# Kernel optimization log

Measured on AMD Instinct MI355X. Metric: run time of the kernel, lower is better.

Reference implementation:

```python
import jax, jax.numpy as jnp
import numpy as np

N = 50000      # nodes
E = 800000     # edges (before self-loops)
IN = 256       # in_channels
HID = 128      # hidden_channels
OUT = 128      # out_channels
NEG_SLOPE = 0.2
EPS = 1e-16


def setup_inputs() -> dict:
    key = jax.random.key(0)
    ks = jax.random.split(key, 16)
    p = lambda k, shape: jax.random.normal(k, shape, jnp.float32) * 0.1
    return {
        "x": jax.random.normal(ks[0], (N, IN), jnp.float32),
        "edge_index": jax.random.randint(ks[1], (2, E), 0, N, dtype=jnp.int64),
        # semantic MLP
        "W1": p(ks[2], (IN, HID)), "b1": jnp.zeros((HID,), jnp.float32),
        "W2": p(ks[3], (HID, HID)), "b2": jnp.zeros((HID,), jnp.float32),
        # gat1: HID -> HID//2, heads=4, concat -> 2*HID
        "g1_W": p(ks[4], (HID, 4 * (HID // 2))),
        "g1_as": p(ks[5], (4, HID // 2)), "g1_ad": p(ks[6], (4, HID // 2)),
        "g1_b": jnp.zeros((4 * (HID // 2),), jnp.float32),
        # gat2: 2*HID -> OUT, heads=2, mean -> OUT
        "g2_W": p(ks[7], (2 * HID, 2 * OUT)),
        "g2_as": p(ks[8], (2, OUT)), "g2_ad": p(ks[9], (2, OUT)),
        "g2_b": jnp.zeros((OUT,), jnp.float32),
        # gat3: OUT -> OUT, heads=1, mean -> OUT
        "g3_W": p(ks[10], (OUT, OUT)),
        "g3_as": p(ks[11], (1, OUT)), "g3_ad": p(ks[12], (1, OUT)),
        "g3_b": jnp.zeros((OUT,), jnp.float32),
    }


def _gat(h_in, src, dst, W, a_src, a_dst, bias, heads, concat, n):
    # Linear projection into heads: [n, H, C]
    h = (h_in @ W).reshape(n, heads, -1)
    alpha_s = jnp.sum(h * a_src[None], axis=-1)  # [n, H]
    alpha_d = jnp.sum(h * a_dst[None], axis=-1)  # [n, H]
    e = jax.nn.leaky_relu(alpha_s[src] + alpha_d[dst], NEG_SLOPE)  # [E', H]
    # segment softmax over edges grouped by destination node
    m = jax.ops.segment_max(e, dst, num_segments=n)
    ex = jnp.exp(e - m[dst])
    denom = jax.ops.segment_sum(ex, dst, num_segments=n)
    alpha = ex / (denom[dst] + EPS)  # [E', H]
    msg = h[src] * alpha[..., None]  # [E', H, C]
    out = jax.ops.segment_sum(msg, dst, num_segments=n)  # [n, H, C]
    out = out.reshape(n, -1) if concat else out.mean(axis=1)
    return out + bias


def reference(x, edge_index, W1, b1, W2, b2,
              g1_W, g1_as, g1_ad, g1_b,
              g2_W, g2_as, g2_ad, g2_b,
              g3_W, g3_as, g3_ad, g3_b):
    n = x.shape[0]
    # PyG GATConv add_self_loops=True: append self-loop edges once
    loops = jnp.arange(n, dtype=edge_index.dtype)
    src = jnp.concatenate([edge_index[0], loops])
    dst = jnp.concatenate([edge_index[1], loops])
    # semantic MLP (inference: dropout = identity)
    h = jax.nn.relu(x @ W1 + b1)
    h = jax.nn.relu(h @ W2 + b2)
    h = jax.nn.elu(_gat(h, src, dst, g1_W, g1_as, g1_ad, g1_b, 4, True, n))
    h = jax.nn.elu(_gat(h, src, dst, g2_W, g2_as, g2_ad, g2_b, 2, False, n))
    h = _gat(h, src, dst, g3_W, g3_as, g3_ad, g3_b, 1, False, n)
    return h
```

## Files before the change

kernel.cpp:

```cpp
#include <hip/hip_runtime.h>
#include <math.h>


#define NEG_SLOPE 0.2f
#define EPS_DEN 1e-16f

typedef __attribute__((ext_vector_type(8))) short short8;
typedef __attribute__((ext_vector_type(4))) float f32x4;
typedef __attribute__((ext_vector_type(4))) unsigned short u16x4;

__device__ inline unsigned short f2b(float f) {
  unsigned u = __builtin_bit_cast(unsigned, f);
  unsigned r = (u + 0x7fffu + ((u >> 16) & 1u)) >> 16;
  return (unsigned short)r;
}
__device__ inline float b2f(unsigned short u) {
  return __builtin_bit_cast(float, (unsigned)u << 16);
}

__device__ inline void glds16(const void* g, void* l) {
  __builtin_amdgcn_global_load_lds(
      (const __attribute__((address_space(1))) void*)g,
      (__attribute__((address_space(3))) void*)l, 16, 0, 0);
}

template <int H>
__device__ inline void loadH(const float* p, float* v) {
  if constexpr (H == 4) {
    float4 t = *(const float4*)p;
    v[0] = t.x; v[1] = t.y; v[2] = t.z; v[3] = t.w;
  } else if constexpr (H == 2) {
    float2 t = *(const float2*)p;
    v[0] = t.x; v[1] = t.y;
  } else {
    v[0] = *p;
  }
}

template <int ACT, int OBF>
__global__ __launch_bounds__(256) void mfma_gemm(
    const unsigned short* __restrict__ A, const unsigned short* __restrict__ Bt,
    const float* __restrict__ bias, float* __restrict__ Cf,
    unsigned short* __restrict__ Cb, int n, int K, int M) {
  __shared__ unsigned short As[128 * 64];
  __shared__ unsigned short Bs[128 * 64];

  const int tid = threadIdx.x;
  const int w = tid >> 6, lane = tid & 63;
  const int row0 = blockIdx.x * 128, col0 = blockIdx.y * 128;
  const int lr = lane >> 3, lg = lane & 7;
  const int lm = lane & 15, kg = lane >> 4;
  const int wm = (w >> 1) * 64, wn = (w & 1) * 64;

  f32x4 acc[4][4];
#pragma unroll
  for (int i = 0; i < 4; i++)
#pragma unroll
    for (int j = 0; j < 4; j++) acc[i][j] = {0.f, 0.f, 0.f, 0.f};

  const int swz = (lg ^ lr) << 3;

  for (int k0 = 0; k0 < K; k0 += 64) {
    __syncthreads();
#pragma unroll
    for (int it = 0; it < 4; it++) {
      const int r = w * 32 + it * 8;
      glds16(A + (size_t)(row0 + r + lr) * K + k0 + swz, &As[r * 64]);
      glds16(Bt + (size_t)(col0 + r + lr) * K + k0 + swz, &Bs[r * 64]);
    }
    __syncthreads();

#pragma unroll
    for (int kh = 0; kh < 2; kh++) {
      const int sw = ((kh * 4 + kg) ^ (lm & 7)) << 3;
      short8 aF[4], bF[4];
#pragma unroll
      for (int i = 0; i < 4; i++) {
        aF[i] = *(const short8*)&As[(wm + i * 16 + lm) * 64 + sw];
        bF[i] = *(const short8*)&Bs[(wn + i * 16 + lm) * 64 + sw];
      }
#pragma unroll
      for (int i = 0; i < 4; i++)
#pragma unroll
        for (int j = 0; j < 4; j++)
          acc[i][j] = __builtin_amdgcn_mfma_f32_16x16x32_bf16(
              aF[i], bF[j], acc[i][j], 0, 0, 0);
    }
  }

  const int r4 = (lane >> 4) * 4;
#pragma unroll
  for (int j = 0; j < 4; j++) {
    const int col = col0 + wn + j * 16 + lm;
    const float bv = bias ? bias[col] : 0.f;
#pragma unroll
    for (int i = 0; i < 4; i++) {
#pragma unroll
      for (int r = 0; r < 4; r++) {
        const int row = row0 + wm + i * 16 + r4 + r;
        if (row < n) {
          float v = acc[i][j][r] + bv;
          if (ACT == 1) v = v > 0.f ? v : 0.f;
          if (OBF)
            Cb[(size_t)row * M + col] = f2b(v);
          else
            Cf[(size_t)row * M + col] = v;
        }
      }
    }
  }
}

struct PrepArgs {
  const float* x; unsigned short* xb; long long nx;
  const float* W[5]; unsigned short* Wt[5];
  int K[5], M[5], t0[6];
  int* deg; int N;
};

__global__ __launch_bounds__(256) void fused_prep_kernel(PrepArgs a) {
  const int tid = threadIdx.x, bid = blockIdx.x, nb = gridDim.x;
  const long long gt = (long long)bid * 256 + tid;
  const long long gsz = (long long)nb * 256;
  __shared__ float tt[32][33];

  for (long long i = gt; i < a.N; i += gsz) a.deg[i] = 0;
  for (long long i = gt * 4; i < a.nx; i += gsz * 4) {
    float4 v = *(const float4*)(a.x + i);
    u16x4 u = {f2b(v.x), f2b(v.y), f2b(v.z), f2b(v.w)};
    *(u16x4*)(a.xb + i) = u;
  }
  for (int t = bid; t < a.t0[5]; t += nb) {
    int di = 0;
    while (t >= a.t0[di + 1]) di++;
    const int local = t - a.t0[di];
    const int K = a.K[di], M = a.M[di], mtiles = M / 32;
    const int mb = (local % mtiles) * 32, kb = (local / mtiles) * 32;
    const float* W = a.W[di];
    unsigned short* Wt = a.Wt[di];
    const int tx = tid & 31, ty = tid >> 5;
    __syncthreads();
#pragma unroll
    for (int i = 0; i < 4; i++)
      tt[ty + i * 8][tx] = W[(size_t)(kb + ty + i * 8) * M + mb + tx];
    __syncthreads();
#pragma unroll
    for (int i = 0; i < 4; i++)
      Wt[(size_t)(mb + ty + i * 8) * K + kb + tx] = f2b(tt[tx][ty + i * 8]);
  }
}

__global__ void count_deg_kernel(const int* __restrict__ edst,
                                 int* __restrict__ deg, int E, int n) {
  int i = blockIdx.x * blockDim.x + threadIdx.x;
  if (i >= E + n) return;
  int d = (i < E) ? edst[i] : (i - E);
  if ((unsigned)d < (unsigned)n) atomicAdd(&deg[d], 1);
}

__global__ __launch_bounds__(256) void block_reduce_kernel(
    const int* __restrict__ deg, int* __restrict__ bsum, int n) {
  __shared__ int s[256];
  const int t = threadIdx.x, i = blockIdx.x * 256 + t;
  s[t] = (i < n) ? deg[i] : 0;
  __syncthreads();
#pragma unroll
  for (int off = 128; off; off >>= 1) {
    if (t < off) s[t] += s[t + off];
    __syncthreads();
  }
  if (t == 0) bsum[blockIdx.x] = s[0];
}

__global__ __launch_bounds__(256) void scan_bsums_kernel(int* __restrict__ bsum,
                                                         int nb) {
  __shared__ int s[256];
  const int t = threadIdx.x;
  const int v = (t < nb) ? bsum[t] : 0;
  s[t] = v;
  __syncthreads();
#pragma unroll
  for (int off = 1; off < 256; off <<= 1) {
    int a = (t >= off) ? s[t - off] : 0;
    __syncthreads();
    s[t] += a;
    __syncthreads();
  }
  if (t < nb) bsum[t] = s[t] - v;
}

__global__ __launch_bounds__(256) void scan_final_kernel(
    const int* __restrict__ deg, const int* __restrict__ bsumx,
    int* __restrict__ rowptr, int* __restrict__ cursor, int n) {
  __shared__ int s[256];
  const int t = threadIdx.x, i = blockIdx.x * 256 + t;
  const int v = (i < n) ? deg[i] : 0;
  s[t] = v;
  __syncthreads();
#pragma unroll
  for (int off = 1; off < 256; off <<= 1) {
    int a = (t >= off) ? s[t - off] : 0;
    __syncthreads();
    s[t] += a;
    __syncthreads();
  }
  if (i < n) {
    const int base = bsumx[blockIdx.x];
    const int excl = base + s[t] - v;
    rowptr[i] = excl;
    cursor[i] = excl;
    if (i == n - 1) rowptr[n] = base + s[t];
  }
}

__global__ void scatter_kernel(const int* __restrict__ esrc,
                               const int* __restrict__ edst,
                               int* __restrict__ cursor,
                               int* __restrict__ csr_src, int E, int n) {
  int i = blockIdx.x * blockDim.x + threadIdx.x;
  int tot = E + n;
  if (i >= tot) return;
  int s, d;
  if (i < E) { s = esrc[i]; d = edst[i]; } else { s = d = i - E; }
  if ((unsigned)d >= (unsigned)n || (unsigned)s >= (unsigned)n) return;
  int pos = atomicAdd(&cursor[d], 1);
  if (pos < tot) csr_src[pos] = s;
}

template <int H, int C>
__global__ __launch_bounds__(256) void alpha_kernel(
    const unsigned short* __restrict__ proj, const float* __restrict__ a_s,
    const float* __restrict__ a_d, float* __restrict__ alpha_s,
    float* __restrict__ alpha_d, int n) {
  constexpr int HC = H * C;
  constexpr int GL = C / 4;
  const int wid = (blockIdx.x * blockDim.x + threadIdx.x) >> 6;
  const int lane = threadIdx.x & 63;
  if (wid >= n) return;
  const int c0 = lane * 4;
  float ps = 0.f, pd = 0.f;
  if (c0 < HC) {
    u16x4 raw = *(const u16x4*)(proj + (size_t)wid * HC + c0);
    float4 as = *(const float4*)(a_s + c0);
    float4 ad = *(const float4*)(a_d + c0);
    float f0 = b2f(raw.x), f1 = b2f(raw.y), f2 = b2f(raw.z), f3 = b2f(raw.w);
    ps = f0 * as.x + f1 * as.y + f2 * as.z + f3 * as.w;
    pd = f0 * ad.x + f1 * ad.y + f2 * ad.z + f3 * ad.w;
  }
#pragma unroll
  for (int off = 1; off < GL; off <<= 1) {
    ps += __shfl_xor(ps, off, 64);
    pd += __shfl_xor(pd, off, 64);
  }
  if (c0 < HC && (lane % GL) == 0) {
    int h = c0 / C;
    alpha_s[(size_t)wid * H + h] = ps;
    alpha_d[(size_t)wid * H + h] = pd;
  }
}

template <int H, int C, bool CONCAT, int ACT, int OBF>
__global__ __launch_bounds__(256) void gat_fused_kernel(
    const unsigned short* __restrict__ proj, const float* __restrict__ alpha_s,
    const float* __restrict__ alpha_d, const int* __restrict__ rowptr,
    const int* __restrict__ csr_src, const float* __restrict__ bias,
    void* __restrict__ out, int n) {
  constexpr int HC = H * C;
  constexpr int ROWSPAN = HC / 8;
  constexpr int EDGES = 64 / ROWSPAN;
  constexpr int WLANES = C / 8;

  __shared__ float exs[4][64 * H];
  __shared__ int sids[4][64];

  const int wv = threadIdx.x >> 6;
  const int wid = (blockIdx.x * blockDim.x + threadIdx.x) >> 6;
  const int lane = threadIdx.x & 63;
  if (wid >= n) return;
  const int dst = wid;
  const int eslot = lane / ROWSPAN;
  const int sl = lane % ROWSPAN;
  const int h_lane = (sl * 8) / C;
  float* myex = &exs[wv][0];
  int* mysid = &sids[wv][0];

  float adv[H];
  loadH<H>(alpha_d + (size_t)dst * H, adv);
  const int rs = rowptr[dst], re = rowptr[dst + 1];

  float denomp[H];
#pragma unroll
  for (int h = 0; h < H; h++) denomp[h] = 0.f;
  float acc[8];
#pragma unroll
  for (int k = 0; k < 8; k++) acc[k] = 0.f;

  for (int base = rs; base < re; base += 64) {
    const int cnt = min(64, re - base);
    if (lane < cnt) {
      const int s = csr_src[base + lane];
      mysid[lane] = s;
      float as[H];
      loadH<H>(alpha_s + (size_t)s * H, as);
#pragma unroll
      for (int h = 0; h < H; h++) {
        float e = as[h] + adv[h];
        e = e > 0.f ? e : NEG_SLOPE * e;
        const float ex = __expf(e);
        denomp[h] += ex;
        myex[lane * H + h] = ex;
      }
    }
    __builtin_amdgcn_wave_barrier();
    int j = eslot;
    for (; j + EDGES < cnt; j += 2 * EDGES) {
      const int s0 = mysid[j];
      const int s1 = mysid[j + EDGES];
      const float w0 = myex[j * H + h_lane];
      const float w1 = myex[(j + EDGES) * H + h_lane];
      const short8 r0 = *(const short8*)(proj + (size_t)s0 * HC + sl * 8);
      const short8 r1 = *(const short8*)(proj + (size_t)s1 * HC + sl * 8);
#pragma unroll
      for (int k = 0; k < 8; k++) acc[k] += w0 * b2f((unsigned short)r0[k]);
#pragma unroll
      for (int k = 0; k < 8; k++) acc[k] += w1 * b2f((unsigned short)r1[k]);
    }
    for (; j < cnt; j += EDGES) {
      const int s0 = mysid[j];
      const float w0 = myex[j * H + h_lane];
      const short8 r0 = *(const short8*)(proj + (size_t)s0 * HC + sl * 8);
#pragma unroll
      for (int k = 0; k < 8; k++) acc[k] += w0 * b2f((unsigned short)r0[k]);
    }
    __builtin_amdgcn_wave_barrier();
  }

#pragma unroll
  for (int off = 32; off; off >>= 1)
#pragma unroll
    for (int h = 0; h < H; h++)
      denomp[h] += __shfl_xor(denomp[h], off, 64);
#pragma unroll
  for (int off = ROWSPAN; off < 64; off <<= 1)
#pragma unroll
    for (int k = 0; k < 8; k++) acc[k] += __shfl_xor(acc[k], off, 64);

  const float inv = 1.f / (denomp[h_lane] + EPS_DEN);
  float v[8];
#pragma unroll
  for (int k = 0; k < 8; k++) v[k] = acc[k] * inv;

  if (!CONCAT && H == 2) {
#pragma unroll
    for (int k = 0; k < 8; k++) v[k] += __shfl_xor(v[k], 16, 64);
  }

  if (CONCAT) {
    if (eslot != 0) return;
    const int c0 = sl * 8;
    float vv[8];
#pragma unroll
    for (int k = 0; k < 8; k++) {
      float t = v[k] + bias[c0 + k];
      if (ACT == 1) t = t > 0.f ? t : (__expf(t) - 1.f);
      vv[k] = t;
    }
    if (OBF) {
      short8 o;
#pragma unroll
      for (int k = 0; k < 8; k++) o[k] = (short)f2b(vv[k]);
      *(short8*)((unsigned short*)out + (size_t)dst * HC + c0) = o;
    } else {
      float* op = (float*)out + (size_t)dst * HC + c0;
      *(float4*)op = make_float4(vv[0], vv[1], vv[2], vv[3]);
      *(float4*)(op + 4) = make_float4(vv[4], vv[5], vv[6], vv[7]);
    }
  } else {
    if (eslot != 0 || sl >= WLANES) return;
    const int c0 = sl * 8;
    const float invH = 1.f / (float)H;
    float vv[8];
#pragma unroll
    for (int k = 0; k < 8; k++) {
      float t = v[k] * invH + bias[c0 + k];
      if (ACT == 1) t = t > 0.f ? t : (__expf(t) - 1.f);
      vv[k] = t;
    }
    if (OBF) {
      short8 o;
#pragma unroll
      for (int k = 0; k < 8; k++) o[k] = (short)f2b(vv[k]);
      *(short8*)((unsigned short*)out + (size_t)dst * C + c0) = o;
    } else {
      float* op = (float*)out + (size_t)dst * C + c0;
      *(float4*)op = make_float4(vv[0], vv[1], vv[2], vv[3]);
      *(float4*)(op + 4) = make_float4(vv[4], vv[5], vv[6], vv[7]);
    }
  }
}

extern "C" void kernel_launch(void* const* d_in, const int* in_sizes, int n_in,
                              void* d_out, int out_size, void* d_ws,
                              size_t ws_size, hipStream_t stream) {
  const float* x    = (const float*)d_in[0];
  const int*   ei   = (const int*)d_in[1];
  const float* W1   = (const float*)d_in[2];
  const float* b1   = (const float*)d_in[3];
  const float* W2   = (const float*)d_in[4];
  const float* b2   = (const float*)d_in[5];
  const float* g1W  = (const float*)d_in[6];
  const float* g1as = (const float*)d_in[7];
  const float* g1ad = (const float*)d_in[8];
  const float* g1b  = (const float*)d_in[9];
  const float* g2W  = (const float*)d_in[10];
  const float* g2as = (const float*)d_in[11];
  const float* g2ad = (const float*)d_in[12];
  const float* g2b  = (const float*)d_in[13];
  const float* g3W  = (const float*)d_in[14];
  const float* g3as = (const float*)d_in[15];
  const float* g3ad = (const float*)d_in[16];
  const float* g3b  = (const float*)d_in[17];

  const int N = in_sizes[0] / 256;
  const int E = in_sizes[1] / 2;
  const int Etot = E + N;
  const int NT = (N + 127) / 128;
  const int NP = NT * 128;
  const int NB = (N + 255) / 256;

  char* p = (char*)d_ws;
  unsigned short* Pb  = (unsigned short*)p; p += (size_t)NP * 256 * 2;
  unsigned short* xb  = (unsigned short*)p; p += (size_t)NP * 256 * 2;
  unsigned short* h1b = (unsigned short*)p; p += (size_t)NP * 128 * 2;
  unsigned short* h2b = (unsigned short*)p; p += (size_t)NP * 128 * 2;
  unsigned short* W1t = (unsigned short*)p; p += (size_t)128 * 256 * 2;
  unsigned short* W2t = (unsigned short*)p; p += (size_t)128 * 128 * 2;
  unsigned short* g1Wt = (unsigned short*)p; p += (size_t)256 * 128 * 2;
  unsigned short* g2Wt = (unsigned short*)p; p += (size_t)256 * 256 * 2;
  unsigned short* g3Wt = (unsigned short*)p; p += (size_t)128 * 128 * 2;
  float* alS  = (float*)p; p += (size_t)N * 4 * 4;
  float* alD  = (float*)p; p += (size_t)N * 4 * 4;
  int* deg    = (int*)p;
  int* rowptr = deg + N;
  int* cursor = rowptr + N + 1;
  int* bsum   = cursor + N;
  int* csrsrc = bsum + 256;

  const int* esrc = ei;
  const int* edst = ei + E;
  unsigned short* act1b = xb;
  unsigned short* act2b = h2b;

  PrepArgs pa;
  pa.x = x; pa.xb = xb; pa.nx = (long long)N * 256;
  pa.W[0] = W1;  pa.Wt[0] = W1t;  pa.K[0] = 256; pa.M[0] = 128;
  pa.W[1] = W2;  pa.Wt[1] = W2t;  pa.K[1] = 128; pa.M[1] = 128;
  pa.W[2] = g1W; pa.Wt[2] = g1Wt; pa.K[2] = 128; pa.M[2] = 256;
  pa.W[3] = g2W; pa.Wt[3] = g2Wt; pa.K[3] = 256; pa.M[3] = 256;
  pa.W[4] = g3W; pa.Wt[4] = g3Wt; pa.K[4] = 128; pa.M[4] = 128;
  pa.t0[0] = 0;
  for (int i = 0; i < 5; i++)
    pa.t0[i + 1] = pa.t0[i] + (pa.K[i] / 32) * (pa.M[i] / 32);
  pa.deg = deg; pa.N = N;
  fused_prep_kernel<<<512, 256, 0, stream>>>(pa);

  count_deg_kernel<<<(Etot + 255) / 256, 256, 0, stream>>>(edst, deg, E, N);
  block_reduce_kernel<<<NB, 256, 0, stream>>>(deg, bsum, N);
  scan_bsums_kernel<<<1, 256, 0, stream>>>(bsum, NB);
  scan_final_kernel<<<NB, 256, 0, stream>>>(deg, bsum, rowptr, cursor, N);
  scatter_kernel<<<(Etot + 255) / 256, 256, 0, stream>>>(esrc, edst, cursor,
                                                         csrsrc, E, N);

  mfma_gemm<1, 1><<<dim3(NT, 1), 256, 0, stream>>>(xb, W1t, b1, nullptr, h1b,
                                                   N, 256, 128);
  mfma_gemm<1, 1><<<dim3(NT, 1), 256, 0, stream>>>(h1b, W2t, b2, nullptr, h2b,
                                                   N, 128, 128);

  mfma_gemm<0, 1><<<dim3(NT, 2), 256, 0, stream>>>(h2b, g1Wt, nullptr, nullptr,
                                                   Pb, N, 128, 256);
  alpha_kernel<4, 64><<<(N + 3) / 4, 256, 0, stream>>>(Pb, g1as, g1ad, alS,
                                                       alD, N);
  gat_fused_kernel<4, 64, true, 1, 1><<<(N + 3) / 4, 256, 0, stream>>>(
      Pb, alS, alD, rowptr, csrsrc, g1b, act1b, N);

  mfma_gemm<0, 1><<<dim3(NT, 2), 256, 0, stream>>>(act1b, g2Wt, nullptr,
                                                   nullptr, Pb, N, 256, 256);
  alpha_kernel<2, 128><<<(N + 3) / 4, 256, 0, stream>>>(Pb, g2as, g2ad, alS,
                                                        alD, N);
  gat_fused_kernel<2, 128, false, 1, 1><<<(N + 3) / 4, 256, 0, stream>>>(
      Pb, alS, alD, rowptr, csrsrc, g2b, act2b, N);

  mfma_gemm<0, 1><<<dim3(NT, 1), 256, 0, stream>>>(act2b, g3Wt, nullptr,
                                                   nullptr, Pb, N, 128, 128);
  alpha_kernel<1, 128><<<(N + 3) / 4, 256, 0, stream>>>(Pb, g3as, g3ad, alS,
                                                        alD, N);
  gat_fused_kernel<1, 128, false, 0, 0><<<(N + 3) / 4, 256, 0, stream>>>(
      Pb, alS, alD, rowptr, csrsrc, g3b, d_out, N);
}
```

Measured before the change: 511.3 us.

## Fuse attention-coefficient dot products into GEMM epilogue and unroll gather loop

Removes the three separate alpha kernels by computing the per-head a_src/a_dst dot products inside the projection GEMM epilogue. Each wave reduces its partial sums with lane shuffles and accumulates them into zero-initialised per-layer buffers with atomics. The buffers are cleared in the prep kernel. The GAT aggregation loop is also unrolled from 2 to 4 edges per iteration to keep more gathers in flight. In exchange, alphas are now computed from fp32 accumulators rather than bf16-rounded values, and the epilogue carries extra shuffles and atomics.

```diff
diff --git a/kernel.cpp b/kernel.cpp
--- a/kernel.cpp
+++ b/kernel.cpp
@@ -37,11 +37,13 @@
   }
 }
 
-template <int ACT, int OBF>
+template <int ACT, int OBF, int ALPHA>
 __global__ __launch_bounds__(256) void mfma_gemm(
     const unsigned short* __restrict__ A, const unsigned short* __restrict__ Bt,
     const float* __restrict__ bias, float* __restrict__ Cf,
-    unsigned short* __restrict__ Cb, int n, int K, int M) {
+    unsigned short* __restrict__ Cb, int n, int K, int M,
+    const float* __restrict__ a_s, const float* __restrict__ a_d,
+    float* __restrict__ alS, float* __restrict__ alD, int Chead, int H) {
   __shared__ unsigned short As[128 * 64];
   __shared__ unsigned short Bs[128 * 64];
 
@@ -88,7 +90,7 @@
     }
   }
 
-  const int r4 = (lane >> 4) * 4;
+  const int r4 = kg * 4;
 #pragma unroll
   for (int j = 0; j < 4; j++) {
     const int col = col0 + wn + j * 16 + lm;
@@ -109,13 +111,45 @@
       }
     }
   }
+
+  if (ALPHA) {
+    const int h = (col0 + wn) / Chead;
+    float asl[4], adl[4];
+#pragma unroll
+    for (int j = 0; j < 4; j++) {
+      asl[j] = a_s[col0 + wn + j * 16 + lm];
+      adl[j] = a_d[col0 + wn + j * 16 + lm];
+    }
+#pragma unroll
+    for (int i = 0; i < 4; i++) {
+#pragma unroll
+      for (int r = 0; r < 4; r++) {
+        float ps = 0.f, pd = 0.f;
+#pragma unroll
+        for (int j = 0; j < 4; j++) {
+          ps += acc[i][j][r] * asl[j];
+          pd += acc[i][j][r] * adl[j];
+        }
+#pragma unroll
+        for (int off = 1; off < 16; off <<= 1) {
+          ps += __shfl_xor(ps, off, 64);
+          pd += __shfl_xor(pd, off, 64);
+        }
+        const int row = row0 + wm + i * 16 + r4 + r;
+        if (lm == 0 && row < n) {
+          atomicAdd(&alS[(size_t)row * H + h], ps);
+          atomicAdd(&alD[(size_t)row * H + h], pd);
+        }
+      }
+    }
+  }
 }
 
 struct PrepArgs {
   const float* x; unsigned short* xb; long long nx;
   const float* W[5]; unsigned short* Wt[5];
   int K[5], M[5], t0[6];
-  int* deg; int N;
+  int* deg; float* alzero; long long nalz; int N;
 };
 
 __global__ __launch_bounds__(256) void fused_prep_kernel(PrepArgs a) {
@@ -125,6 +159,7 @@
   __shared__ float tt[32][33];
 
   for (long long i = gt; i < a.N; i += gsz) a.deg[i] = 0;
+  for (long long i = gt; i < a.nalz; i += gsz) a.alzero[i] = 0.f;
   for (long long i = gt * 4; i < a.nx; i += gsz * 4) {
     float4 v = *(const float4*)(a.x + i);
     u16x4 u = {f2b(v.x), f2b(v.y), f2b(v.z), f2b(v.w)};
@@ -227,38 +262,6 @@
   if (pos < tot) csr_src[pos] = s;
 }
 
-template <int H, int C>
-__global__ __launch_bounds__(256) void alpha_kernel(
-    const unsigned short* __restrict__ proj, const float* __restrict__ a_s,
-    const float* __restrict__ a_d, float* __restrict__ alpha_s,
-    float* __restrict__ alpha_d, int n) {
-  constexpr int HC = H * C;
-  constexpr int GL = C / 4;
-  const int wid = (blockIdx.x * blockDim.x + threadIdx.x) >> 6;
-  const int lane = threadIdx.x & 63;
-  if (wid >= n) return;
-  const int c0 = lane * 4;
-  float ps = 0.f, pd = 0.f;
-  if (c0 < HC) {
-    u16x4 raw = *(const u16x4*)(proj + (size_t)wid * HC + c0);
-    float4 as = *(const float4*)(a_s + c0);
-    float4 ad = *(const float4*)(a_d + c0);
-    float f0 = b2f(raw.x), f1 = b2f(raw.y), f2 = b2f(raw.z), f3 = b2f(raw.w);
-    ps = f0 * as.x + f1 * as.y + f2 * as.z + f3 * as.w;
-    pd = f0 * ad.x + f1 * ad.y + f2 * ad.z + f3 * ad.w;
-  }
-#pragma unroll
-  for (int off = 1; off < GL; off <<= 1) {
-    ps += __shfl_xor(ps, off, 64);
-    pd += __shfl_xor(pd, off, 64);
-  }
-  if (c0 < HC && (lane % GL) == 0) {
-    int h = c0 / C;
-    alpha_s[(size_t)wid * H + h] = ps;
-    alpha_d[(size_t)wid * H + h] = pd;
-  }
-}
-
 template <int H, int C, bool CONCAT, int ACT, int OBF>
 __global__ __launch_bounds__(256) void gat_fused_kernel(
     const unsigned short* __restrict__ proj, const float* __restrict__ alpha_s,
@@ -313,17 +316,23 @@
     }
     __builtin_amdgcn_wave_barrier();
     int j = eslot;
-    for (; j + EDGES < cnt; j += 2 * EDGES) {
-      const int s0 = mysid[j];
-      const int s1 = mysid[j + EDGES];
-      const float w0 = myex[j * H + h_lane];
-      const float w1 = myex[(j + EDGES) * H + h_lane];
-      const short8 r0 = *(const short8*)(proj + (size_t)s0 * HC + sl * 8);
-      const short8 r1 = *(const short8*)(proj + (size_t)s1 * HC + sl * 8);
-#pragma unroll
-      for (int k = 0; k < 8; k++) acc[k] += w0 * b2f((unsigned short)r0[k]);
-#pragma unroll
-      for (int k = 0; k < 8; k++) acc[k] += w1 * b2f((unsigned short)r1[k]);
+    for (; j + 3 * EDGES < cnt; j += 4 * EDGES) {
+      int ss[4];
+      float ww[4];
+      short8 rr[4];
+#pragma unroll
+      for (int q = 0; q < 4; q++) {
+        ss[q] = mysid[j + q * EDGES];
+        ww[q] = myex[(j + q * EDGES) * H + h_lane];
+      }
+#pragma unroll
+      for (int q = 0; q < 4; q++)
+        rr[q] = *(const short8*)(proj + (size_t)ss[q] * HC + sl * 8);
+#pragma unroll
+      for (int q = 0; q < 4; q++)
+#pragma unroll
+        for (int k = 0; k < 8; k++)
+          acc[k] += ww[q] * b2f((unsigned short)rr[q][k]);
     }
     for (; j < cnt; j += EDGES) {
       const int s0 = mysid[j];
@@ -438,8 +447,12 @@
   unsigned short* g1Wt = (unsigned short*)p; p += (size_t)256 * 128 * 2;
   unsigned short* g2Wt = (unsigned short*)p; p += (size_t)256 * 256 * 2;
   unsigned short* g3Wt = (unsigned short*)p; p += (size_t)128 * 128 * 2;
-  float* alS  = (float*)p; p += (size_t)N * 4 * 4;
-  float* alD  = (float*)p; p += (size_t)N * 4 * 4;
+  float* alS1 = (float*)p; p += (size_t)NP * 4 * 4;
+  float* alD1 = (float*)p; p += (size_t)NP * 4 * 4;
+  float* alS2 = (float*)p; p += (size_t)NP * 2 * 4;
+  float* alD2 = (float*)p; p += (size_t)NP * 2 * 4;
+  float* alS3 = (float*)p; p += (size_t)NP * 1 * 4;
+  float* alD3 = (float*)p; p += (size_t)NP * 1 * 4;
   int* deg    = (int*)p;
   int* rowptr = deg + N;
   int* cursor = rowptr + N + 1;
@@ -450,6 +463,7 @@
   const int* edst = ei + E;
   unsigned short* act1b = xb;
   unsigned short* act2b = h2b;
+  const long long nalz = (long long)NP * (4 + 4 + 2 + 2 + 1 + 1);
 
   PrepArgs pa;
   pa.x = x; pa.xb = xb; pa.nx = (long long)N * 256;
@@ -461,7 +475,7 @@
   pa.t0[0] = 0;
   for (int i = 0; i < 5; i++)
     pa.t0[i + 1] = pa.t0[i] + (pa.K[i] / 32) * (pa.M[i] / 32);
-  pa.deg = deg; pa.N = N;
+  pa.deg = deg; pa.alzero = alS1; pa.nalz = nalz; pa.N = N;
   fused_prep_kernel<<<512, 256, 0, stream>>>(pa);
 
   count_deg_kernel<<<(Etot + 255) / 256, 256, 0, stream>>>(edst, deg, E, N);
@@ -471,29 +485,28 @@
   scatter_kernel<<<(Etot + 255) / 256, 256, 0, stream>>>(esrc, edst, cursor,
                                                          csrsrc, E, N);
 
-  mfma_gemm<1, 1><<<dim3(NT, 1), 256, 0, stream>>>(xb, W1t, b1, nullptr, h1b,
-                                                   N, 256, 128);
-  mfma_gemm<1, 1><<<dim3(NT, 1), 256, 0, stream>>>(h1b, W2t, b2, nullptr, h2b,
-                                                   N, 128, 128);
-
-  mfma_gemm<0, 1><<<dim3(NT, 2), 256, 0, stream>>>(h2b, g1Wt, nullptr, nullptr,
-                                                   Pb, N, 128, 256);
-  alpha_kernel<4, 64><<<(N + 3) / 4, 256, 0, stream>>>(Pb, g1as, g1ad, alS,
-                                                       alD, N);
+  mfma_gemm<1, 1, 0><<<dim3(NT, 1), 256, 0, stream>>>(
+      xb, W1t, b1, nullptr, h1b, N, 256, 128, nullptr, nullptr, nullptr,
+      nullptr, 0, 0);
+  mfma_gemm<1, 1, 0><<<dim3(NT, 1), 256, 0, stream>>>(
+      h1b, W2t, b2, nullptr, h2b, N, 128, 128, nullptr, nullptr, nullptr,
+      nullptr, 0, 0);
+
+  mfma_gemm<0, 1, 1><<<dim3(NT, 2), 256, 0, stream>>>(
+      h2b, g1Wt, nullptr, nullptr, Pb, N, 128, 256, g1as, g1ad, alS1, alD1,
+      64, 4);
   gat_fused_kernel<4, 64, true, 1, 1><<<(N + 3) / 4, 256, 0, stream>>>(
-      Pb, alS, alD, rowptr, csrsrc, g1b, act1b, N);
-
-  mfma_gemm<0, 1><<<dim3(NT, 2), 256, 0, stream>>>(act1b, g2Wt, nullptr,
-                                                   nullptr, Pb, N, 256, 256);
-  alpha_kernel<2, 128><<<(N + 3) / 4, 256, 0, stream>>>(Pb, g2as, g2ad, alS,
-                                                        alD, N);
+      Pb, alS1, alD1, rowptr, csrsrc, g1b, act1b, N);
+
+  mfma_gemm<0, 1, 1><<<dim3(NT, 2), 256, 0, stream>>>(
+      act1b, g2Wt, nullptr, nullptr, Pb, N, 256, 256, g2as, g2ad, alS2, alD2,
+      128, 2);
   gat_fused_kernel<2, 128, false, 1, 1><<<(N + 3) / 4, 256, 0, stream>>>(
-      Pb, alS, alD, rowptr, csrsrc, g2b, act2b, N);
-
-  mfma_gemm<0, 1><<<dim3(NT, 1), 256, 0, stream>>>(act2b, g3Wt, nullptr,
-                                                   nullptr, Pb, N, 128, 128);
-  alpha_kernel<1, 128><<<(N + 3) / 4, 256, 0, stream>>>(Pb, g3as, g3ad, alS,
-                                                        alD, N);
+      Pb, alS2, alD2, rowptr, csrsrc, g2b, act2b, N);
+
+  mfma_gemm<0, 1, 1><<<dim3(NT, 1), 256, 0, stream>>>(
+      act2b, g3Wt, nullptr, nullptr, Pb, N, 128, 128, g3as, g3ad, alS3, alD3,
+      128, 1);
   gat_fused_kernel<1, 128, false, 0, 0><<<(N + 3) / 4, 256, 0, stream>>>(
-      Pb, alS, alD, rowptr, csrsrc, g3b, d_out, N);
-}
+      Pb, alS3, alD3, rowptr, csrsrc, g3b, d_out, N);
+}
```

After: 526.6 us. 3.0% more time.
